# Optimization experiments

Measured on AMD Instinct MI355X. Metric: run time of the kernel, lower is better.

## Reference

```python
import jax, jax.numpy as jnp
import numpy as np

EMBED_DIM = 512
NUM_HEADS = 8
HEAD_DIM = EMBED_DIM // NUM_HEADS


def setup_inputs() -> dict:
    key = jax.random.key(0)
    ks = jax.random.split(key, 6)
    B, S, D = 2, 4096, EMBED_DIM
    scale = 1.0 / np.sqrt(D)
    inputs = jax.random.normal(ks[0], (B, S, D), dtype=jnp.float32)
    Wq = jax.random.normal(ks[1], (D, D), dtype=jnp.float32) * scale
    Wk = jax.random.normal(ks[2], (D, D), dtype=jnp.float32) * scale
    Wv = jax.random.normal(ks[3], (D, D), dtype=jnp.float32) * scale
    Wo = jax.random.normal(ks[4], (D, D), dtype=jnp.float32) * scale
    zeros = jnp.zeros((D,), dtype=jnp.float32)
    return {"inputs": inputs, "Wq": Wq, "bq": zeros, "Wk": Wk, "bk": zeros,
            "Wv": Wv, "bv": zeros, "Wo": Wo, "bo": zeros}


def _split_heads(x, B, S):
    # [B,S,D] -> [B,H,S,hd]
    return x.reshape(B, S, NUM_HEADS, HEAD_DIM).transpose(0, 2, 1, 3)


def reference(inputs, Wq, bq, Wk, bk, Wv, bv, Wo, bo):
    B, S, D = inputs.shape
    q = _split_heads(inputs @ Wq + bq, B, S)
    k = _split_heads(inputs @ Wk + bk, B, S)
    v = _split_heads(inputs @ Wv + bv, B, S)
    scale = 1.0 / jnp.sqrt(jnp.asarray(HEAD_DIM, dtype=inputs.dtype))
    # full [B,H,S,S] score matrix, as in the original naive SDPA
    scores = jnp.einsum('bhqd,bhkd->bhqk', q, k) * scale
    weights = jax.nn.softmax(scores, axis=-1)
    attn = jnp.einsum('bhqk,bhkd->bhqd', weights, v)
    attn = attn.transpose(0, 2, 1, 3).reshape(B, S, D)
    return attn @ Wo + bo
```

## Files before the change

### kernel.cpp

```cpp
#include <hip/hip_runtime.h>
#include <hip/hip_bf16.h>
#include <stdint.h>


typedef __bf16 bf16x8 __attribute__((ext_vector_type(8)));
typedef float f32x4 __attribute__((ext_vector_type(4)));

using as1_void = __attribute__((address_space(1))) void;
using as3_void = __attribute__((address_space(3))) void;

__device__ __forceinline__ void gload16(const void* g, void* l) {
    __builtin_amdgcn_global_load_lds((const as1_void*)g, (as3_void*)l, 16, 0, 0);
}

__device__ __forceinline__ f32x4 mfma16(bf16x8 a, bf16x8 b, f32x4 c) {
    return __builtin_amdgcn_mfma_f32_16x16x32_bf16(a, b, c, 0, 0, 0);
}

__device__ __forceinline__ uint32_t pkbf(float a, float b) {
    union { __hip_bfloat16 h[2]; uint32_t u; } r;
    r.h[0] = __float2bfloat16(a);
    r.h[1] = __float2bfloat16(b);
    return r.u;
}

__global__ void cvt_x(const float* __restrict__ in, __hip_bfloat16* __restrict__ out, int n) {
    int i = (blockIdx.x * 256 + threadIdx.x) * 4;
    if (i >= n) return;
    float4 v = *reinterpret_cast<const float4*>(in + i);
    union { __hip_bfloat16 h[4]; uint2 u; } r;
    r.h[0] = __float2bfloat16(v.x);
    r.h[1] = __float2bfloat16(v.y);
    r.h[2] = __float2bfloat16(v.z);
    r.h[3] = __float2bfloat16(v.w);
    *reinterpret_cast<uint2*>(out + i) = r.u;
}

__global__ void cvt_wt(const float* __restrict__ w0, const float* __restrict__ w1,
                       const float* __restrict__ w2, const float* __restrict__ w3,
                       __hip_bfloat16* __restrict__ o0, __hip_bfloat16* __restrict__ o1,
                       __hip_bfloat16* __restrict__ o2, __hip_bfloat16* __restrict__ o3) {
    const float* W; __hip_bfloat16* O;
    switch (blockIdx.z) {
        case 0: W = w0; O = o0; break;
        case 1: W = w1; O = o1; break;
        case 2: W = w2; O = o2; break;
        default: W = w3; O = o3; break;
    }
    __shared__ float t[32][33];
    int n0 = blockIdx.x * 32, k0 = blockIdx.y * 32;
    int tx = threadIdx.x, ty = threadIdx.y;
    for (int j = 0; j < 4; ++j)
        t[ty + 8 * j][tx] = W[(size_t)(k0 + ty + 8 * j) * 512 + n0 + tx];
    __syncthreads();
    for (int j = 0; j < 4; ++j)
        O[(size_t)(n0 + ty + 8 * j) * 512 + k0 + tx] = __float2bfloat16(t[tx][ty + 8 * j]);
}

__global__ __launch_bounds__(256, 2) void gemm_qkv(
    const __hip_bfloat16* __restrict__ A, const __hip_bfloat16* __restrict__ Bt,
    const float* __restrict__ bq, const float* __restrict__ bk, const float* __restrict__ bv,
    __hip_bfloat16* __restrict__ Qb, __hip_bfloat16* __restrict__ Kb,
    __hip_bfloat16* __restrict__ Vtb, float qs)
{
    const int K = 512;
    __shared__ __hip_bfloat16 Abuf[128 * 32];
    __shared__ __hip_bfloat16 Bbuf[128 * 32];
    const int tid = threadIdx.x, w = tid >> 6, lane = tid & 63;
    const int col = lane & 15, quad = lane >> 4;
    const int wr = w >> 1, wc = w & 1;
    const int tileN = blockIdx.x * 128, tileM = blockIdx.y * 128;

    f32x4 acc[4][4] = {};

    for (int k0 = 0; k0 < K; k0 += 32) {
        for (int i = 0; i < 2; ++i) {
            int g = w * 2 + i;
            int chunk = g * 64 + lane;
            int row = chunk >> 2, c8 = chunk & 3;
            gload16(A + (size_t)(tileM + row) * K + k0 + c8 * 8, Abuf + g * 512);
            gload16(Bt + (size_t)(tileN + row) * K + k0 + c8 * 8, Bbuf + g * 512);
        }
        __syncthreads();
        bf16x8 af[4], bfr[4];
        for (int mt = 0; mt < 4; ++mt)
            af[mt] = *reinterpret_cast<const bf16x8*>(Abuf + (wr * 64 + mt * 16 + col) * 32 + quad * 8);
        for (int nt = 0; nt < 4; ++nt)
            bfr[nt] = *reinterpret_cast<const bf16x8*>(Bbuf + (wc * 64 + nt * 16 + col) * 32 + quad * 8);
        for (int mt = 0; mt < 4; ++mt)
            for (int nt = 0; nt < 4; ++nt)
                acc[mt][nt] = mfma16(af[mt], bfr[nt], acc[mt][nt]);
        __syncthreads();
    }

    const int seg = (tileN + wc * 64) >> 9;
    const float* bias = (seg == 0) ? bq : (seg == 1) ? bk : bv;
    const float scale = (seg == 0) ? qs : 1.0f;
    __hip_bfloat16* outp = (seg == 0) ? Qb : (seg == 1) ? Kb : Vtb;

    for (int mt = 0; mt < 4; ++mt) {
        for (int nt = 0; nt < 4; ++nt) {
            int n = tileN + wc * 64 + nt * 16 + col;
            int nn = n & 511, h = nn >> 6, d = nn & 63;
            float bn = bias[nn];
            for (int r = 0; r < 4; ++r) {
                int m = tileM + wr * 64 + mt * 16 + quad * 4 + r;
                int b = m >> 12, s = m & 4095;
                float v = (acc[mt][nt][r] + bn) * scale;
                size_t off;
                if (seg < 2) off = (((size_t)(b * 8 + h) * 4096 + s) << 6) + d;
                else         off = (((size_t)(b * 8 + h) * 64 + d) << 12) + s;
                outp[off] = __float2bfloat16(v);
            }
        }
    }
}

__global__ __launch_bounds__(256, 2) void gemm_out(
    const __hip_bfloat16* __restrict__ A, const __hip_bfloat16* __restrict__ Bt,
    const float* __restrict__ bias, float* __restrict__ out)
{
    const int N = 512, K = 512;
    __shared__ __hip_bfloat16 Abuf[128 * 32];
    __shared__ __hip_bfloat16 Bbuf[128 * 32];
    const int tid = threadIdx.x, w = tid >> 6, lane = tid & 63;
    const int col = lane & 15, quad = lane >> 4;
    const int wr = w >> 1, wc = w & 1;
    const int tileN = blockIdx.x * 128, tileM = blockIdx.y * 128;

    f32x4 acc[4][4] = {};

    for (int k0 = 0; k0 < K; k0 += 32) {
        for (int i = 0; i < 2; ++i) {
            int g = w * 2 + i;
            int chunk = g * 64 + lane;
            int row = chunk >> 2, c8 = chunk & 3;
            gload16(A + (size_t)(tileM + row) * K + k0 + c8 * 8, Abuf + g * 512);
            gload16(Bt + (size_t)(tileN + row) * K + k0 + c8 * 8, Bbuf + g * 512);
        }
        __syncthreads();
        bf16x8 af[4], bfr[4];
        for (int mt = 0; mt < 4; ++mt)
            af[mt] = *reinterpret_cast<const bf16x8*>(Abuf + (wr * 64 + mt * 16 + col) * 32 + quad * 8);
        for (int nt = 0; nt < 4; ++nt)
            bfr[nt] = *reinterpret_cast<const bf16x8*>(Bbuf + (wc * 64 + nt * 16 + col) * 32 + quad * 8);
        for (int mt = 0; mt < 4; ++mt)
            for (int nt = 0; nt < 4; ++nt)
                acc[mt][nt] = mfma16(af[mt], bfr[nt], acc[mt][nt]);
        __syncthreads();
    }

    for (int mt = 0; mt < 4; ++mt) {
        for (int nt = 0; nt < 4; ++nt) {
            int n = tileN + wc * 64 + nt * 16 + col;
            float bn = bias[n];
            for (int r = 0; r < 4; ++r) {
                int m = tileM + wr * 64 + mt * 16 + quad * 4 + r;
                out[(size_t)m * N + n] = acc[mt][nt][r] + bn;
            }
        }
    }
}

__global__ __launch_bounds__(256) void flash(
    const __hip_bfloat16* __restrict__ Q,
    const __hip_bfloat16* __restrict__ Kq,
    const __hip_bfloat16* __restrict__ Vt,
    __hip_bfloat16* __restrict__ attnb)
{
    __shared__ __hip_bfloat16 KT[2][4096];
    __shared__ __hip_bfloat16 VB[2][4096];
    __shared__ uint32_t TB[4][1024];

    const int bh = blockIdx.y, b = bh >> 3, h = bh & 7;
    const int tid = threadIdx.x, w = tid >> 6, lane = tid & 63;
    const int col = lane & 15, quad = lane >> 4;
    const int q0 = blockIdx.x * 128 + w * 32;
    const int c7 = col & 7;

    const __hip_bfloat16* Qh = Q + (size_t)bh * 4096 * 64;
    const __hip_bfloat16* Kh = Kq + (size_t)bh * 4096 * 64;
    const __hip_bfloat16* Vh = Vt + (size_t)bh * 64 * 4096;

    bf16x8 aq[2][2];
    for (int qh = 0; qh < 2; ++qh)
        for (int ks = 0; ks < 2; ++ks)
            aq[qh][ks] = *reinterpret_cast<const bf16x8*>(
                Qh + (size_t)(q0 + qh * 16 + col) * 64 + ks * 32 + quad * 8);

    const __hip_bfloat16* ksrc[2];
    const __hip_bfloat16* vsrc[2];
    int ldsoff[2];
    for (int i = 0; i < 2; ++i) {
        int c = i * 256 + tid;
        int row = c >> 3, s8 = (c & 7) ^ (row & 7);
        ksrc[i] = Kh + row * 64 + s8 * 8;
        vsrc[i] = Vh + (size_t)row * 4096 + s8 * 8;
        ldsoff[i] = (i * 256 + w * 64) * 8;
    }

    bf16x8 ones;
    for (int j = 0; j < 8; ++j) ones[j] = (__bf16)1.0f;

    f32x4 o[4][2] = {};
    f32x4 accl[2] = {};

    uint32_t* TBw = &TB[w][0];

    for (int i = 0; i < 2; ++i) {
        gload16(ksrc[i], &KT[0][ldsoff[i]]);
        gload16(vsrc[i], &VB[0][ldsoff[i]]);
    }
    __syncthreads();

    for (int kt = 0; kt < 64; ++kt) {
        const int p = kt & 1;
        if (kt < 63) {
            for (int i = 0; i < 2; ++i) {
                gload16(ksrc[i] + (size_t)(kt + 1) * 4096, &KT[1 - p][ldsoff[i]]);
                gload16(vsrc[i] + (size_t)(kt + 1) * 64,   &VB[1 - p][ldsoff[i]]);
            }
        }

        f32x4 sc[4][2] = {};
        for (int ks = 0; ks < 2; ++ks)
            for (int kg = 0; kg < 4; ++kg) {
                bf16x8 ak = *reinterpret_cast<const bf16x8*>(
                    &KT[p][(kg * 16 + col) * 64 + (((ks * 4 + quad) ^ c7) << 3)]);
                for (int qh = 0; qh < 2; ++qh)
                    sc[kg][qh] = mfma16(ak, aq[qh][ks], sc[kg][qh]);
            }

        for (int kg = 0; kg < 4; ++kg)
            for (int qh = 0; qh < 2; ++qh) {
                f32x4 v = sc[kg][qh];
                uint32_t u0 = pkbf(__builtin_amdgcn_exp2f(v[0]), __builtin_amdgcn_exp2f(v[1]));
                uint32_t u1 = pkbf(__builtin_amdgcn_exp2f(v[2]), __builtin_amdgcn_exp2f(v[3]));
                int q = qh * 16 + col;
                int base = q * 32 + (((kg * 2 + (quad >> 1)) ^ c7) << 2) + ((quad & 1) * 2);
                TBw[base]     = u0;
                TBw[base + 1] = u1;
            }

        bf16x8 bp[2][2];
        for (int qh = 0; qh < 2; ++qh)
            for (int ks = 0; ks < 2; ++ks) {
                int q = qh * 16 + col;
                bp[qh][ks] = *reinterpret_cast<const bf16x8*>(
                    &TBw[q * 32 + (((ks * 4 + quad) ^ c7) << 2)]);
            }

        for (int ks = 0; ks < 2; ++ks) {
            for (int dt = 0; dt < 4; ++dt) {
                bf16x8 av = *reinterpret_cast<const bf16x8*>(
                    &VB[p][(dt * 16 + col) * 64 + (((ks * 4 + quad) ^ c7) << 3)]);
                for (int qh = 0; qh < 2; ++qh)
                    o[dt][qh] = mfma16(av, bp[qh][ks], o[dt][qh]);
            }
            for (int qh = 0; qh < 2; ++qh)
                accl[qh] = mfma16(ones, bp[qh][ks], accl[qh]);
        }

        __syncthreads();
    }

    for (int qh = 0; qh < 2; ++qh) {
        float inv = 1.0f / accl[qh][0];
        int s = q0 + qh * 16 + col;
        __hip_bfloat16* dst = attnb + ((size_t)b * 4096 + s) * 512 + h * 64 + quad * 4;
        for (int dt = 0; dt < 4; ++dt) {
            union { __hip_bfloat16 hh[4]; ushort4 v4; } pk;
            for (int r = 0; r < 4; ++r)
                pk.hh[r] = __float2bfloat16(o[dt][qh][r] * inv);
            *reinterpret_cast<ushort4*>(dst + dt * 16) = pk.v4;
        }
    }
}

extern "C" void kernel_launch(void* const* d_in, const int* in_sizes, int n_in,
                              void* d_out, int out_size, void* d_ws, size_t ws_size,
                              hipStream_t stream) {
    const float* X  = (const float*)d_in[0];
    const float* Wq = (const float*)d_in[1];
    const float* bq = (const float*)d_in[2];
    const float* Wk = (const float*)d_in[3];
    const float* bk = (const float*)d_in[4];
    const float* Wv = (const float*)d_in[5];
    const float* bv = (const float*)d_in[6];
    const float* Wo = (const float*)d_in[7];
    const float* bo = (const float*)d_in[8];
    float* out = (float*)d_out;

    char* ws = (char*)d_ws;
    __hip_bfloat16* Xb  = (__hip_bfloat16*)(ws);
    __hip_bfloat16* Wqt = (__hip_bfloat16*)(ws + ((size_t)8 << 20));
    __hip_bfloat16* Wkt = Wqt + 512 * 512;
    __hip_bfloat16* Wvt = Wkt + 512 * 512;
    __hip_bfloat16* Wot = Wvt + 512 * 512;
    __hip_bfloat16* Qb  = (__hip_bfloat16*)(ws + ((size_t)10 << 20));
    __hip_bfloat16* Kb  = (__hip_bfloat16*)(ws + ((size_t)18 << 20));
    __hip_bfloat16* Vtb = (__hip_bfloat16*)(ws + ((size_t)26 << 20));
    __hip_bfloat16* Atb = (__hip_bfloat16*)(ws + ((size_t)34 << 20));

    const int M = 8192, K = 512;

    cvt_x<<<4096, 256, 0, stream>>>(X, Xb, M * K);
    cvt_wt<<<dim3(16, 16, 4), dim3(32, 8), 0, stream>>>(Wq, Wk, Wv, Wo, Wqt, Wkt, Wvt, Wot);

    const float qs = 0.125f * 1.4426950408889634f;
    gemm_qkv<<<dim3(12, 64), 256, 0, stream>>>(Xb, Wqt, bq, bk, bv, Qb, Kb, Vtb, qs);

    flash<<<dim3(32, 16), 256, 0, stream>>>(Qb, Kb, Vtb, Atb);

    gemm_out<<<dim3(4, 64), 256, 0, stream>>>(Atb, Wot, bo, out);
}
```

Measured before the change: 238.3 us.

## Software-pipeline QK^T one tile ahead of softmax and PV in attention loop

Restructures the attention inner loop so the QK^T MFMAs for tile kt+1 are issued while exp/pack and PV MFMAs run on tile kt. K is prefetched two tiles ahead and V one ahead, with register double-buffered score accumulators, and the loop is unrolled by two via a macro so buffer indices are compile-time constants. P stores are widened to 64-bit LDS writes. The aim is to hide exp latency and LDS waits behind matrix work, at the cost of more registers, which may lower occupancy.

```diff
diff --git a/kernel.cpp b/kernel.cpp
--- a/kernel.cpp
+++ b/kernel.cpp
@@ -204,65 +204,115 @@
 
     f32x4 o[4][2] = {};
     f32x4 accl[2] = {};
+    f32x4 sc[2][4][2];
 
     uint32_t* TBw = &TB[w][0];
-
-    for (int i = 0; i < 2; ++i) {
-        gload16(ksrc[i], &KT[0][ldsoff[i]]);
-        gload16(vsrc[i], &VB[0][ldsoff[i]]);
-    }
+    uint2* TBw2 = reinterpret_cast<uint2*>(TBw);
+
+    gload16(ksrc[0], &KT[0][ldsoff[0]]);
+    gload16(ksrc[1], &KT[0][ldsoff[1]]);
+    gload16(vsrc[0], &VB[0][ldsoff[0]]);
+    gload16(vsrc[1], &VB[0][ldsoff[1]]);
+    gload16(ksrc[0] + 4096, &KT[1][ldsoff[0]]);
+    gload16(ksrc[1] + 4096, &KT[1][ldsoff[1]]);
     __syncthreads();
 
-    for (int kt = 0; kt < 64; ++kt) {
-        const int p = kt & 1;
-        if (kt < 63) {
-            for (int i = 0; i < 2; ++i) {
-                gload16(ksrc[i] + (size_t)(kt + 1) * 4096, &KT[1 - p][ldsoff[i]]);
-                gload16(vsrc[i] + (size_t)(kt + 1) * 64,   &VB[1 - p][ldsoff[i]]);
-            }
-        }
-
-        f32x4 sc[4][2] = {};
-        for (int ks = 0; ks < 2; ++ks)
-            for (int kg = 0; kg < 4; ++kg) {
-                bf16x8 ak = *reinterpret_cast<const bf16x8*>(
-                    &KT[p][(kg * 16 + col) * 64 + (((ks * 4 + quad) ^ c7) << 3)]);
-                for (int qh = 0; qh < 2; ++qh)
-                    sc[kg][qh] = mfma16(ak, aq[qh][ks], sc[kg][qh]);
-            }
-
+    for (int kg = 0; kg < 4; ++kg)
+        for (int qh = 0; qh < 2; ++qh)
+            sc[0][kg][qh] = (f32x4){0.f, 0.f, 0.f, 0.f};
+    for (int ks = 0; ks < 2; ++ks)
+        for (int kg = 0; kg < 4; ++kg) {
+            bf16x8 ak = *reinterpret_cast<const bf16x8*>(
+                &KT[0][(kg * 16 + col) * 64 + (((ks * 4 + quad) ^ c7) << 3)]);
+            for (int qh = 0; qh < 2; ++qh)
+                sc[0][kg][qh] = mfma16(ak, aq[qh][ks], sc[0][kg][qh]);
+        }
+    __syncthreads();
+
+#define FLASH_BODY(KT_, P_)                                                     \
+    {                                                                           \
+        const int kt_ = (KT_);                                                  \
+        int kk = kt_ + 2; if (kk > 63) kk = 63;     \
+        gload16(ksrc[0] + (size_t)kk * 4096, &KT[(P_)][ldsoff[0]]);             \
+        gload16(ksrc[1] + (size_t)kk * 4096, &KT[(P_)][ldsoff[1]]);             \
+        gload16(vsrc[0] + (size_t)(kt_ + 1) * 64, &VB[1 - (P_)][ldsoff[0]]);    \
+        gload16(vsrc[1] + (size_t)(kt_ + 1) * 64, &VB[1 - (P_)][ldsoff[1]]);    \
+                           \
+        for (int kg = 0; kg < 4; ++kg)                                          \
+            for (int qh = 0; qh < 2; ++qh) {                                    \
+                f32x4 v = sc[(P_)][kg][qh];                                     \
+                uint2 u;                                                        \
+                u.x = pkbf(__builtin_amdgcn_exp2f(v[0]),                        \
+                           __builtin_amdgcn_exp2f(v[1]));                       \
+                u.y = pkbf(__builtin_amdgcn_exp2f(v[2]),                        \
+                           __builtin_amdgcn_exp2f(v[3]));                       \
+                TBw2[(qh * 16 + col) * 16 +                                     \
+                     (((kg * 2 + (quad >> 1)) ^ c7) << 1) + (quad & 1)] = u;    \
+            }                                                                   \
+              \
+        for (int kg = 0; kg < 4; ++kg)                                          \
+            for (int qh = 0; qh < 2; ++qh)                                      \
+                sc[1 - (P_)][kg][qh] = (f32x4){0.f, 0.f, 0.f, 0.f};             \
+        for (int ks = 0; ks < 2; ++ks)                                          \
+            for (int kg = 0; kg < 4; ++kg) {                                    \
+                bf16x8 ak = *reinterpret_cast<const bf16x8*>(                   \
+                    &KT[1 - (P_)][(kg * 16 + col) * 64 +                        \
+                                  (((ks * 4 + quad) ^ c7) << 3)]);              \
+                for (int qh = 0; qh < 2; ++qh)                                  \
+                    sc[1 - (P_)][kg][qh] =                                      \
+                        mfma16(ak, aq[qh][ks], sc[1 - (P_)][kg][qh]);           \
+            }                                                                   \
+                                                    \
+        bf16x8 bp[2][2];                                                        \
+        for (int qh = 0; qh < 2; ++qh)                                          \
+            for (int ks = 0; ks < 2; ++ks)                                      \
+                bp[qh][ks] = *reinterpret_cast<const bf16x8*>(                  \
+                    &TBw[(qh * 16 + col) * 32 + (((ks * 4 + quad) ^ c7) << 2)]);\
+        for (int ks = 0; ks < 2; ++ks) {                                        \
+            for (int dt = 0; dt < 4; ++dt) {                                    \
+                bf16x8 av = *reinterpret_cast<const bf16x8*>(                   \
+                    &VB[(P_)][(dt * 16 + col) * 64 +                            \
+                              (((ks * 4 + quad) ^ c7) << 3)]);                  \
+                for (int qh = 0; qh < 2; ++qh)                                  \
+                    o[dt][qh] = mfma16(av, bp[qh][ks], o[dt][qh]);              \
+            }                                                                   \
+            accl[0] = mfma16(ones, bp[0][ks], accl[0]);                         \
+            accl[1] = mfma16(ones, bp[1][ks], accl[1]);                         \
+        }                                                                       \
+        __syncthreads();                                                        \
+    }
+
+    FLASH_BODY(0, 0)
+    for (int kth = 0; kth < 31; ++kth) {
+        FLASH_BODY(2 * kth + 1, 1)
+        FLASH_BODY(2 * kth + 2, 0)
+    }
+    {
         for (int kg = 0; kg < 4; ++kg)
             for (int qh = 0; qh < 2; ++qh) {
-                f32x4 v = sc[kg][qh];
-                uint32_t u0 = pkbf(__builtin_amdgcn_exp2f(v[0]), __builtin_amdgcn_exp2f(v[1]));
-                uint32_t u1 = pkbf(__builtin_amdgcn_exp2f(v[2]), __builtin_amdgcn_exp2f(v[3]));
-                int q = qh * 16 + col;
-                int base = q * 32 + (((kg * 2 + (quad >> 1)) ^ c7) << 2) + ((quad & 1) * 2);
-                TBw[base]     = u0;
-                TBw[base + 1] = u1;
+                f32x4 v = sc[1][kg][qh];
+                uint2 u;
+                u.x = pkbf(__builtin_amdgcn_exp2f(v[0]), __builtin_amdgcn_exp2f(v[1]));
+                u.y = pkbf(__builtin_amdgcn_exp2f(v[2]), __builtin_amdgcn_exp2f(v[3]));
+                TBw2[(qh * 16 + col) * 16 + (((kg * 2 + (quad >> 1)) ^ c7) << 1) + (quad & 1)] = u;
             }
-
         bf16x8 bp[2][2];
         for (int qh = 0; qh < 2; ++qh)
-            for (int ks = 0; ks < 2; ++ks) {
-                int q = qh * 16 + col;
+            for (int ks = 0; ks < 2; ++ks)
                 bp[qh][ks] = *reinterpret_cast<const bf16x8*>(
-                    &TBw[q * 32 + (((ks * 4 + quad) ^ c7) << 2)]);
-            }
-
+                    &TBw[(qh * 16 + col) * 32 + (((ks * 4 + quad) ^ c7) << 2)]);
         for (int ks = 0; ks < 2; ++ks) {
             for (int dt = 0; dt < 4; ++dt) {
                 bf16x8 av = *reinterpret_cast<const bf16x8*>(
-                    &VB[p][(dt * 16 + col) * 64 + (((ks * 4 + quad) ^ c7) << 3)]);
+                    &VB[1][(dt * 16 + col) * 64 + (((ks * 4 + quad) ^ c7) << 3)]);
                 for (int qh = 0; qh < 2; ++qh)
                     o[dt][qh] = mfma16(av, bp[qh][ks], o[dt][qh]);
             }
-            for (int qh = 0; qh < 2; ++qh)
-                accl[qh] = mfma16(ones, bp[qh][ks], accl[qh]);
-        }
-
-        __syncthreads();
-    }
+            accl[0] = mfma16(ones, bp[0][ks], accl[0]);
+            accl[1] = mfma16(ones, bp[1][ks], accl[1]);
+        }
+    }
+#undef FLASH_BODY
 
     for (int qh = 0; qh < 2; ++qh) {
         float inv = 1.0f / accl[qh][0];
```

New measurement: 217.3 us. 8.8% less time.

## Split flash KV range across two wave groups and halve gemm_out N tile

Applied to the files above, without the earlier changes.

The flash kernel now runs 512 threads per block, and two groups of four waves each process half of the key/value sequence (split-K) for the same 128 queries. Partial outputs and row sums are merged through LDS at the end. This doubles the waves resident per CU without adding blocks. The main loop is manually unrolled by two with compile-time buffer parity, and the P tile exchange uses 8-byte stores. Separately, gemm_out uses 128x64 tiles instead of 128x128, giving twice as many blocks for better CU coverage. In exchange there is more LDS per block, a final reduction step, and lower reuse per gemm_out tile.

```diff
diff --git a/kernel.cpp b/kernel.cpp
--- a/kernel.cpp
+++ b/kernel.cpp
@@ -122,13 +122,12 @@
 {
     const int N = 512, K = 512;
     __shared__ __hip_bfloat16 Abuf[128 * 32];
-    __shared__ __hip_bfloat16 Bbuf[128 * 32];
+    __shared__ __hip_bfloat16 Bbuf[64 * 32];
     const int tid = threadIdx.x, w = tid >> 6, lane = tid & 63;
     const int col = lane & 15, quad = lane >> 4;
-    const int wr = w >> 1, wc = w & 1;
-    const int tileN = blockIdx.x * 128, tileM = blockIdx.y * 128;
-
-    f32x4 acc[4][4] = {};
+    const int tileN = blockIdx.x * 64, tileM = blockIdx.y * 128;
+
+    f32x4 acc[2][4] = {};
 
     for (int k0 = 0; k0 < K; k0 += 32) {
         for (int i = 0; i < 2; ++i) {
@@ -136,51 +135,55 @@
             int chunk = g * 64 + lane;
             int row = chunk >> 2, c8 = chunk & 3;
             gload16(A + (size_t)(tileM + row) * K + k0 + c8 * 8, Abuf + g * 512);
-            gload16(Bt + (size_t)(tileN + row) * K + k0 + c8 * 8, Bbuf + g * 512);
+        }
+        {
+            int row = tid >> 2, c8 = tid & 3;
+            gload16(Bt + (size_t)(tileN + row) * K + k0 + c8 * 8, Bbuf + tid * 8);
         }
         __syncthreads();
-        bf16x8 af[4], bfr[4];
-        for (int mt = 0; mt < 4; ++mt)
-            af[mt] = *reinterpret_cast<const bf16x8*>(Abuf + (wr * 64 + mt * 16 + col) * 32 + quad * 8);
+        bf16x8 af[2], bfr[4];
+        for (int mt = 0; mt < 2; ++mt)
+            af[mt] = *reinterpret_cast<const bf16x8*>(Abuf + (w * 32 + mt * 16 + col) * 32 + quad * 8);
         for (int nt = 0; nt < 4; ++nt)
-            bfr[nt] = *reinterpret_cast<const bf16x8*>(Bbuf + (wc * 64 + nt * 16 + col) * 32 + quad * 8);
-        for (int mt = 0; mt < 4; ++mt)
+            bfr[nt] = *reinterpret_cast<const bf16x8*>(Bbuf + (nt * 16 + col) * 32 + quad * 8);
+        for (int mt = 0; mt < 2; ++mt)
             for (int nt = 0; nt < 4; ++nt)
                 acc[mt][nt] = mfma16(af[mt], bfr[nt], acc[mt][nt]);
         __syncthreads();
     }
 
-    for (int mt = 0; mt < 4; ++mt) {
+    for (int mt = 0; mt < 2; ++mt) {
         for (int nt = 0; nt < 4; ++nt) {
-            int n = tileN + wc * 64 + nt * 16 + col;
+            int n = tileN + nt * 16 + col;
             float bn = bias[n];
             for (int r = 0; r < 4; ++r) {
-                int m = tileM + wr * 64 + mt * 16 + quad * 4 + r;
+                int m = tileM + w * 32 + mt * 16 + quad * 4 + r;
                 out[(size_t)m * N + n] = acc[mt][nt][r] + bn;
             }
         }
     }
 }
 
-__global__ __launch_bounds__(256) void flash(
+__global__ __launch_bounds__(512, 4) void flash(
     const __hip_bfloat16* __restrict__ Q,
     const __hip_bfloat16* __restrict__ Kq,
     const __hip_bfloat16* __restrict__ Vt,
     __hip_bfloat16* __restrict__ attnb)
 {
-    __shared__ __hip_bfloat16 KT[2][4096];
-    __shared__ __hip_bfloat16 VB[2][4096];
-    __shared__ uint32_t TB[4][1024];
+    __shared__ __hip_bfloat16 KT[2][2][4096];
+    __shared__ __hip_bfloat16 VB[2][2][4096];
+    __shared__ uint32_t TB[8][512];
 
     const int bh = blockIdx.y, b = bh >> 3, h = bh & 7;
     const int tid = threadIdx.x, w = tid >> 6, lane = tid & 63;
+    const int g = w >> 2, wg = w & 3;
     const int col = lane & 15, quad = lane >> 4;
-    const int q0 = blockIdx.x * 128 + w * 32;
+    const int q0 = blockIdx.x * 128 + wg * 32;
     const int c7 = col & 7;
 
     const __hip_bfloat16* Qh = Q + (size_t)bh * 4096 * 64;
-    const __hip_bfloat16* Kh = Kq + (size_t)bh * 4096 * 64;
-    const __hip_bfloat16* Vh = Vt + (size_t)bh * 64 * 4096;
+    const __hip_bfloat16* Kh = Kq + (size_t)bh * 4096 * 64 + (size_t)g * 2048 * 64;
+    const __hip_bfloat16* Vh = Vt + (size_t)bh * 64 * 4096 + (size_t)g * 2048;
 
     bf16x8 aq[2][2];
     for (int qh = 0; qh < 2; ++qh)
@@ -192,11 +195,11 @@
     const __hip_bfloat16* vsrc[2];
     int ldsoff[2];
     for (int i = 0; i < 2; ++i) {
-        int c = i * 256 + tid;
+        int c = i * 256 + wg * 64 + lane;
         int row = c >> 3, s8 = (c & 7) ^ (row & 7);
         ksrc[i] = Kh + row * 64 + s8 * 8;
         vsrc[i] = Vh + (size_t)row * 4096 + s8 * 8;
-        ldsoff[i] = (i * 256 + w * 64) * 8;
+        ldsoff[i] = (i * 256 + wg * 64) * 8;
     }
 
     bf16x8 ones;
@@ -204,75 +207,115 @@
 
     f32x4 o[4][2] = {};
     f32x4 accl[2] = {};
+    f32x4 sc[4][2];
 
     uint32_t* TBw = &TB[w][0];
-
-    for (int i = 0; i < 2; ++i) {
-        gload16(ksrc[i], &KT[0][ldsoff[i]]);
-        gload16(vsrc[i], &VB[0][ldsoff[i]]);
-    }
+    uint2* TBw2 = reinterpret_cast<uint2*>(TBw);
+
+#define SOFTMAX_STORE(QH_)                                                      \
+    for (int kg = 0; kg < 4; ++kg) {                                            \
+        f32x4 v = sc[kg][(QH_)];                                                \
+        uint2 u;                                                                \
+        u.x = pkbf(__builtin_amdgcn_exp2f(v[0]), __builtin_amdgcn_exp2f(v[1])); \
+        u.y = pkbf(__builtin_amdgcn_exp2f(v[2]), __builtin_amdgcn_exp2f(v[3])); \
+        TBw2[col * 16 + (((kg * 2 + (quad >> 1)) ^ c7) << 1) + (quad & 1)] = u; \
+    }
+#define BP_READ(QH_)                                                            \
+    for (int ks = 0; ks < 2; ++ks)                                              \
+        bp[(QH_)][ks] = *reinterpret_cast<const bf16x8*>(                       \
+            &TBw[col * 32 + (((ks * 4 + quad) ^ c7) << 2)]);
+
+#define QK_TILE(P_)                                                             \
+    for (int kg = 0; kg < 4; ++kg)                                              \
+        for (int qh = 0; qh < 2; ++qh)                                          \
+            sc[kg][qh] = (f32x4){0.f, 0.f, 0.f, 0.f};                           \
+    for (int ks = 0; ks < 2; ++ks)                                              \
+        for (int kg = 0; kg < 4; ++kg) {                                        \
+            bf16x8 ak = *reinterpret_cast<const bf16x8*>(                       \
+                &KT[g][(P_)][(kg * 16 + col) * 64 + (((ks * 4 + quad) ^ c7) << 3)]); \
+            for (int qh = 0; qh < 2; ++qh)                                      \
+                sc[kg][qh] = mfma16(ak, aq[qh][ks], sc[kg][qh]);                \
+        }
+
+#define PV_TILE(P_)                                                             \
+    for (int ks = 0; ks < 2; ++ks) {                                            \
+        for (int dt = 0; dt < 4; ++dt) {                                        \
+            bf16x8 av = *reinterpret_cast<const bf16x8*>(                       \
+                &VB[g][(P_)][(dt * 16 + col) * 64 + (((ks * 4 + quad) ^ c7) << 3)]); \
+            for (int qh = 0; qh < 2; ++qh)                                      \
+                o[dt][qh] = mfma16(av, bp[qh][ks], o[dt][qh]);                  \
+        }                                                                       \
+        accl[0] = mfma16(ones, bp[0][ks], accl[0]);                             \
+        accl[1] = mfma16(ones, bp[1][ks], accl[1]);                             \
+    }
+
+#define FLASH_BODY(KT_, P_)                                                     \
+    {                                                                           \
+        const int kt_ = (KT_);                                                  \
+        gload16(ksrc[0] + (size_t)(kt_ + 1) * 4096, &KT[g][1 - (P_)][ldsoff[0]]); \
+        gload16(ksrc[1] + (size_t)(kt_ + 1) * 4096, &KT[g][1 - (P_)][ldsoff[1]]); \
+        gload16(vsrc[0] + (size_t)(kt_ + 1) * 64, &VB[g][1 - (P_)][ldsoff[0]]); \
+        gload16(vsrc[1] + (size_t)(kt_ + 1) * 64, &VB[g][1 - (P_)][ldsoff[1]]); \
+        QK_TILE(P_)                                                             \
+        bf16x8 bp[2][2];                                                        \
+        SOFTMAX_STORE(0) BP_READ(0) SOFTMAX_STORE(1) BP_READ(1)                 \
+        PV_TILE(P_)                                                             \
+        __syncthreads();                                                        \
+    }
+
+    gload16(ksrc[0], &KT[g][0][ldsoff[0]]);
+    gload16(ksrc[1], &KT[g][0][ldsoff[1]]);
+    gload16(vsrc[0], &VB[g][0][ldsoff[0]]);
+    gload16(vsrc[1], &VB[g][0][ldsoff[1]]);
     __syncthreads();
 
-    for (int kt = 0; kt < 64; ++kt) {
-        const int p = kt & 1;
-        if (kt < 63) {
-            for (int i = 0; i < 2; ++i) {
-                gload16(ksrc[i] + (size_t)(kt + 1) * 4096, &KT[1 - p][ldsoff[i]]);
-                gload16(vsrc[i] + (size_t)(kt + 1) * 64,   &VB[1 - p][ldsoff[i]]);
+    FLASH_BODY(0, 0)
+    for (int kth = 0; kth < 15; ++kth) {
+        FLASH_BODY(2 * kth + 1, 1)
+        FLASH_BODY(2 * kth + 2, 0)
+    }
+    {
+        QK_TILE(1)
+        bf16x8 bp[2][2];
+        SOFTMAX_STORE(0) BP_READ(0) SOFTMAX_STORE(1) BP_READ(1)
+        PV_TILE(1)
+    }
+#undef FLASH_BODY
+#undef QK_TILE
+#undef PV_TILE
+#undef SOFTMAX_STORE
+#undef BP_READ
+
+    __syncthreads();
+    float* MB = reinterpret_cast<float*>(&KT[0][0][0]);
+    float* Lb = reinterpret_cast<float*>(&TB[0][0]);
+    if (g == 1) {
+        float* M = MB + wg * 2048;
+        for (int qh = 0; qh < 2; ++qh)
+            for (int dt = 0; dt < 4; ++dt)
+                *reinterpret_cast<f32x4*>(
+                    M + (qh * 16 + col) * 64 + (((dt * 4 + quad) ^ col) << 2)) = o[dt][qh];
+        if (quad == 0) {
+            Lb[wg * 32 + col]      = accl[0][0];
+            Lb[wg * 32 + 16 + col] = accl[1][0];
+        }
+    }
+    __syncthreads();
+    if (g == 0) {
+        float* M = MB + wg * 2048;
+        for (int qh = 0; qh < 2; ++qh) {
+            float l = accl[qh][0] + Lb[wg * 32 + qh * 16 + col];
+            float inv = 1.0f / l;
+            int s = q0 + qh * 16 + col;
+            __hip_bfloat16* dst = attnb + ((size_t)b * 4096 + s) * 512 + h * 64 + quad * 4;
+            for (int dt = 0; dt < 4; ++dt) {
+                f32x4 p = o[dt][qh] + *reinterpret_cast<const f32x4*>(
+                    M + (qh * 16 + col) * 64 + (((dt * 4 + quad) ^ col) << 2));
+                union { __hip_bfloat16 hh[4]; ushort4 v4; } pk;
+                for (int r = 0; r < 4; ++r)
+                    pk.hh[r] = __float2bfloat16(p[r] * inv);
+                *reinterpret_cast<ushort4*>(dst + dt * 16) = pk.v4;
             }
-        }
-
-        f32x4 sc[4][2] = {};
-        for (int ks = 0; ks < 2; ++ks)
-            for (int kg = 0; kg < 4; ++kg) {
-                bf16x8 ak = *reinterpret_cast<const bf16x8*>(
-                    &KT[p][(kg * 16 + col) * 64 + (((ks * 4 + quad) ^ c7) << 3)]);
-                for (int qh = 0; qh < 2; ++qh)
-                    sc[kg][qh] = mfma16(ak, aq[qh][ks], sc[kg][qh]);
-            }
-
-        for (int kg = 0; kg < 4; ++kg)
-            for (int qh = 0; qh < 2; ++qh) {
-                f32x4 v = sc[kg][qh];
-                uint32_t u0 = pkbf(__builtin_amdgcn_exp2f(v[0]), __builtin_amdgcn_exp2f(v[1]));
-                uint32_t u1 = pkbf(__builtin_amdgcn_exp2f(v[2]), __builtin_amdgcn_exp2f(v[3]));
-                int q = qh * 16 + col;
-                int base = q * 32 + (((kg * 2 + (quad >> 1)) ^ c7) << 2) + ((quad & 1) * 2);
-                TBw[base]     = u0;
-                TBw[base + 1] = u1;
-            }
-
-        bf16x8 bp[2][2];
-        for (int qh = 0; qh < 2; ++qh)
-            for (int ks = 0; ks < 2; ++ks) {
-                int q = qh * 16 + col;
-                bp[qh][ks] = *reinterpret_cast<const bf16x8*>(
-                    &TBw[q * 32 + (((ks * 4 + quad) ^ c7) << 2)]);
-            }
-
-        for (int ks = 0; ks < 2; ++ks) {
-            for (int dt = 0; dt < 4; ++dt) {
-                bf16x8 av = *reinterpret_cast<const bf16x8*>(
-                    &VB[p][(dt * 16 + col) * 64 + (((ks * 4 + quad) ^ c7) << 3)]);
-                for (int qh = 0; qh < 2; ++qh)
-                    o[dt][qh] = mfma16(av, bp[qh][ks], o[dt][qh]);
-            }
-            for (int qh = 0; qh < 2; ++qh)
-                accl[qh] = mfma16(ones, bp[qh][ks], accl[qh]);
-        }
-
-        __syncthreads();
-    }
-
-    for (int qh = 0; qh < 2; ++qh) {
-        float inv = 1.0f / accl[qh][0];
-        int s = q0 + qh * 16 + col;
-        __hip_bfloat16* dst = attnb + ((size_t)b * 4096 + s) * 512 + h * 64 + quad * 4;
-        for (int dt = 0; dt < 4; ++dt) {
-            union { __hip_bfloat16 hh[4]; ushort4 v4; } pk;
-            for (int r = 0; r < 4; ++r)
-                pk.hh[r] = __float2bfloat16(o[dt][qh][r] * inv);
-            *reinterpret_cast<ushort4*>(dst + dt * 16) = pk.v4;
         }
     }
 }
@@ -310,7 +353,7 @@
     const float qs = 0.125f * 1.4426950408889634f;
     gemm_qkv<<<dim3(12, 64), 256, 0, stream>>>(Xb, Wqt, bq, bk, bv, Qb, Kb, Vtb, qs);
 
-    flash<<<dim3(32, 16), 256, 0, stream>>>(Qb, Kb, Vtb, Atb);
-
-    gemm_out<<<dim3(4, 64), 256, 0, stream>>>(Atb, Wot, bo, out);
-}
+    flash<<<dim3(32, 16), 512, 0, stream>>>(Qb, Kb, Vtb, Atb);
+
+    gemm_out<<<dim3(8, 64), 256, 0, stream>>>(Atb, Wot, bo, out);
+}
```

After: 238.1 us. About the same (-0.1%).
